# Performance work log

Measured on AMD Instinct MI355X. Metric: run time of the kernel, lower is better.

## Reference

```python
import jax, jax.numpy as jnp
import numpy as np

IN, H, L, B, S = 512, 1024, 6, 64, 256


def setup_inputs() -> dict:
    key = jax.random.key(0)
    ks = jax.random.split(key, 8)
    stdv = 1.0 / np.sqrt(H)
    u = lambda k, shp: jax.random.uniform(k, shp, jnp.float32, -stdv, stdv)
    x = jax.random.normal(ks[0], (B, S, IN), jnp.float32)
    # gate order along last axis of 4H: i, f, c(g), o
    U0 = u(ks[1], (IN, 4 * H))   # layer 0 input weights
    V0 = u(ks[2], (H, 4 * H))    # layer 0 recurrent weights
    b0 = u(ks[3], (4 * H,))
    U = u(ks[4], (L - 1, H, 4 * H))  # layers 1..L-1 input weights
    V = u(ks[5], (L - 1, H, 4 * H))
    b = u(ks[6], (L - 1, 4 * H))
    return {"x": x, "U0": U0, "V0": V0, "b0": b0, "U": U, "V": V, "b": b}


def _cell(xt, h, c, Um, Vm, bm):
    # fused 4-gate GEMM: [B, in] @ [in, 4H] + [B, H] @ [H, 4H]
    z = xt @ Um + h @ Vm + bm
    i, f, g, o = jnp.split(z, 4, axis=-1)
    i = jax.nn.sigmoid(i)
    f = jax.nn.sigmoid(f)
    g = jnp.tanh(g)
    o = jax.nn.sigmoid(o)
    c = f * c + i * g
    h = o * jnp.tanh(c)
    return h, c


def reference(x, U0, V0, b0, U, V, b):
    # Dropout is identity in eval mode (faithful to module.eval()).
    Bb = x.shape[0]
    h0 = jnp.zeros((L, Bb, H), x.dtype)
    c0 = jnp.zeros((L, Bb, H), x.dtype)

    def step(carry, xt):
        h, c = carry
        hs, cs = [], []
        inp = xt
        hn, cn = _cell(inp, h[0], c[0], U0, V0, b0)
        hs.append(hn); cs.append(cn); inp = hn
        for l in range(L - 1):  # fixed small layer loop
            hn, cn = _cell(inp, h[l + 1], c[l + 1], U[l], V[l], b[l])
            hs.append(hn); cs.append(cn); inp = hn
        return (jnp.stack(hs), jnp.stack(cs)), inp

    (hf, cf), seq = jax.lax.scan(step, (h0, c0), jnp.swapaxes(x, 0, 1))
    hidden_seq = jnp.swapaxes(seq, 0, 1)  # [B, S, H]
    return hidden_seq, hf, cf
```

## Files before the change

### kernel.cpp

```cpp
#include <hip/hip_runtime.h>
#include <hip/hip_cooperative_groups.h>

#define B_ 64
#define H_ 1024
#define IN_ 512
#define S_ 256
#define L_ 6
#define NG_ 4096
#define NTASK 768
#define NTICK (S_ + L_ - 1)

typedef __bf16 bf16x8 __attribute__((ext_vector_type(8)));
typedef float f32x4 __attribute__((ext_vector_type(4)));
typedef unsigned short ushort8v __attribute__((ext_vector_type(8)));
typedef unsigned short ushort_t;

#define WP_BYTES 96468992ul
#define XB_BYTES 16777216ul
#define HBF_ELEMS 786432ul
#define LSLOT 65536ul
#define XSLOT 32768ul

__host__ __device__ __forceinline__ size_t poff(int l, int jb) {
  return (l == 0) ? (size_t)jb * 49152ul
                  : 6291456ul + ((size_t)(l - 1) * 128 + jb) * 65536ul;
}

#define MFMA16(a, b, c) __builtin_amdgcn_mfma_f32_16x16x32_bf16(a, b, c, 0, 0, 0)
#define WAITN(n) asm volatile("s_waitcnt vmcnt(" #n ")" ::: "memory")
#define SB0() __builtin_amdgcn_sched_barrier(0)

__device__ __forceinline__ unsigned short f2bf(float f) {
  union { float f; unsigned u; } v; v.f = f;
  unsigned r = v.u + 0x7fffu + ((v.u >> 16) & 1u);
  return (unsigned short)(r >> 16);
}

__global__ void k_pack_w(const float* __restrict__ U0, const float* __restrict__ V0,
                         const float* __restrict__ U, const float* __restrict__ V,
                         ushort_t* __restrict__ Wp) {
  const int bx = blockIdx.x;
  const int l = bx >> 7, jb = bx & 127;
  ushort_t* __restrict__ panel = Wp + poff(l, jb);
  const int KU = (l == 0) ? IN_ : H_;
  const int NU = KU >> 6;
  const int NCH = NU + 16;
  const float* __restrict__ Usrc = (l == 0) ? U0 : U + (size_t)(l - 1) * H_ * NG_;
  const float* __restrict__ Vsrc = (l == 0) ? V0 : V + (size_t)(l - 1) * H_ * NG_;
  const int t = threadIdx.x, lane = t & 63, g4 = t >> 6;
  const int l15 = lane & 15, kg = lane >> 4;
  for (int p = 0; p < NCH; ++p) {
    const int gi = p * 4 + g4;
    const int c = gi >> 2, u = gi & 3, nf = u >> 1, ks = u & 1;
    const int n = (nf * 2 + (l15 >> 3)) * 1024 + jb * 8 + (l15 & 7);
    const int k = c * 64 + ks * 32 + kg * 8;
    const float* __restrict__ src =
        (c < NU) ? (Usrc + (size_t)k * NG_ + n)
                 : (Vsrc + (size_t)(k - KU) * NG_ + n);
    ushort8v uv;
#pragma unroll
    for (int e = 0; e < 8; ++e) uv[e] = f2bf(src[(size_t)e * NG_]);
    *(ushort8v*)(panel + (size_t)gi * 512 + lane * 8) = uv;
  }
}

__global__ void k_cvt_x(const float* __restrict__ x, ushort_t* __restrict__ xb) {
  const int tt = blockIdx.x;
  const int tid = threadIdx.x;
  const int b = tid >> 2, kq = (tid & 3) << 7;
  const float* __restrict__ src = x + ((size_t)b * S_ + tt) * IN_ + kq;
  ushort_t* __restrict__ dst = xb + (size_t)tt * XSLOT;
  const int w = b >> 4, l15 = b & 15;
#pragma unroll
  for (int kk = 0; kk < 128; kk += 8) {
    float4 v0 = *(const float4*)(src + kk);
    float4 v1 = *(const float4*)(src + kk + 4);
    ushort8v u = { f2bf(v0.x), f2bf(v0.y), f2bf(v0.z), f2bf(v0.w),
                   f2bf(v1.x), f2bf(v1.y), f2bf(v1.z), f2bf(v1.w) };
    const int k = kq + kk;
    const int ks = k >> 5, kg = (k & 31) >> 3;
    *(ushort8v*)(dst + (((size_t)ks * 4 + w) * 64 + kg * 16 + l15) * 8) = u;
  }
}

template<int NCH>
__device__ __forceinline__ void gemm_tick(f32x4 acc[2],
                                          const ushort_t* __restrict__ panel,
                                          const ushort_t* __restrict__ A1,
                                          const ushort_t* __restrict__ A2,
                                          int w, int lane) {
  constexpr int NU = NCH - 16;
  bf16x8 Wb[3][4];
  bf16x8 Ab[3][2];
#define LDU(p) (*(const bf16x8*)(p))
#define ISSUE(c) do { \
    const ushort_t* wp_ = panel + (size_t)(c) * 2048 + lane * 8; \
    Wb[(c) % 3][0] = LDU(wp_); \
    Wb[(c) % 3][1] = LDU(wp_ + 512); \
    Wb[(c) % 3][2] = LDU(wp_ + 1024); \
    Wb[(c) % 3][3] = LDU(wp_ + 1536); \
    const ushort_t* ap_ = ((c) < NU \
        ? A1 + ((size_t)(2 * (c)) * 4 + w) * 512 \
        : A2 + ((size_t)(2 * ((c) - NU)) * 4 + w) * 512) + lane * 8; \
    Ab[(c) % 3][0] = LDU(ap_); \
    Ab[(c) % 3][1] = LDU(ap_ + 2048); \
  } while (0)
  ISSUE(0); ISSUE(1); ISSUE(2);
  SB0();
#pragma unroll
  for (int c = 0; c < NCH; ++c) {
    const int rem = NCH - 1 - c;
    if (rem >= 2) { WAITN(12); }
    else if (rem == 1) { WAITN(6); }
    else { WAITN(0); }
    SB0();
    acc[0] = MFMA16(Ab[c % 3][0], Wb[c % 3][0], acc[0]);
    acc[1] = MFMA16(Ab[c % 3][0], Wb[c % 3][2], acc[1]);
    acc[0] = MFMA16(Ab[c % 3][1], Wb[c % 3][1], acc[0]);
    acc[1] = MFMA16(Ab[c % 3][1], Wb[c % 3][3], acc[1]);
    SB0();
    if (c + 3 < NCH) ISSUE(c + 3);
    SB0();
  }
#undef ISSUE
#undef LDU
}

__global__ void __launch_bounds__(256, 3)
k_lstm(const ushort_t* __restrict__ xb,
       const ushort_t* __restrict__ Wp,
       const float* __restrict__ b0,
       const float* __restrict__ bL,
       ushort_t* __restrict__ hbf,
       float* __restrict__ out, int multi) {
  cooperative_groups::grid_group grid = cooperative_groups::this_grid();
  float* __restrict__ seq = out;
  float* __restrict__ hf = out + (size_t)B_ * S_ * H_;
  float* __restrict__ cf = hf + (size_t)L_ * B_ * H_;
  __shared__ float hstF[512];

  const int tid = threadIdx.x;
  const int w = tid >> 6;
  const int lane = tid & 63;
  const int l15 = lane & 15;
  const int kg = lane >> 4;
  const bool lo = (l15 < 8);
  const int wg = blockIdx.x;
  const int nwg = gridDim.x;

  float creg[4] = {0.f, 0.f, 0.f, 0.f};

  for (int T = 0; T < NTICK; ++T) {
    for (int task = wg; task < NTASK; task += nwg) {
      const int l = task >> 7;
      const int jb = task & 127;
      const int t = T - l;
      if (t < 0 || t >= S_) continue;
      const ushort_t* __restrict__ hprev = hbf + (size_t)((T + 1) & 1) * (L_ * LSLOT);
      ushort_t* __restrict__ hcur = hbf + (size_t)(T & 1) * (L_ * LSLOT);
      const ushort_t* __restrict__ panel = Wp + poff(l, jb);
      const ushort_t* __restrict__ A2 = hprev + (size_t)l * LSLOT;

      f32x4 acc[2];
      acc[0] = (f32x4){0.f, 0.f, 0.f, 0.f};
      acc[1] = (f32x4){0.f, 0.f, 0.f, 0.f};
      if (l == 0)
        gemm_tick<24>(acc, panel, xb + (size_t)t * XSLOT, A2, w, lane);
      else
        gemm_tick<32>(acc, panel, hprev + (size_t)(l - 1) * LSLOT, A2, w, lane);

      const int hc = (jb << 3) + (l15 & 7);
      const float* __restrict__ bias = (l == 0) ? b0 : (bL + (size_t)(l - 1) * NG_);
      const float bi = bias[hc];
      const float bfv = bias[1024 + hc];
      const float bgv = bias[2048 + hc];
      const float bov = bias[3072 + hc];

#pragma unroll
      for (int j = 0; j < 4; ++j) {
        float a0 = acc[0][j], a1 = acc[1][j];
        float p0 = __shfl_xor(a0, 8, 64);
        float p1 = __shfl_xor(a1, 8, 64);
        float zi = (lo ? a0 : p0) + bi;
        float zf = (lo ? p0 : a0) + bfv;
        float zg = (lo ? a1 : p1) + bgv;
        float zo = (lo ? p1 : a1) + bov;
        float iv = 1.f / (1.f + expf(-zi));
        float fv = 1.f / (1.f + expf(-zf));
        float gv = tanhf(zg);
        float ov = 1.f / (1.f + expf(-zo));
        const int r = w * 16 + kg * 4 + j;
        float cold;
        if (multi)
          cold = (t > 0) ? cf[((size_t)l * B_ + r) * H_ + hc] : 0.f;
        else
          cold = creg[j];
        float cn = fv * cold + iv * gv;
        creg[j] = cn;
        float hv = ov * tanhf(cn);
        if (lo) {
          hstF[w * 128 + (kg * 4 + j) * 8 + l15] = hv;
          if (multi || t == S_ - 1) cf[((size_t)l * B_ + r) * H_ + hc] = cn;
          if (t == S_ - 1) hf[((size_t)l * B_ + r) * H_ + hc] = hv;
        }
      }
      __syncthreads();
      if (kg == 0) {
        const int lr = l15;
        float4 v0 = *(const float4*)&hstF[w * 128 + lr * 8];
        float4 v1 = *(const float4*)&hstF[w * 128 + lr * 8 + 4];
        ushort8v u8 = { f2bf(v0.x), f2bf(v0.y), f2bf(v0.z), f2bf(v0.w),
                        f2bf(v1.x), f2bf(v1.y), f2bf(v1.z), f2bf(v1.w) };
        *(ushort8v*)(hcur + (size_t)l * LSLOT +
                     (((size_t)(jb >> 2) * 4 + w) * 64 + (jb & 3) * 16 + lr) * 8) = u8;
        if (l == L_ - 1) {
          float* sp = seq + (((size_t)(w * 16 + lr)) * S_ + t) * H_ + (jb << 3);
          *(float4*)sp = v0;
          *(float4*)(sp + 4) = v1;
        }
      }
      __syncthreads();
    }
    grid.sync();
  }
}

extern "C" void kernel_launch(void* const* d_in, const int* in_sizes, int n_in,
                              void* d_out, int out_size, void* d_ws, size_t ws_size,
                              hipStream_t stream) {
  const float* x = (const float*)d_in[0];
  const float* U0 = (const float*)d_in[1];
  const float* V0 = (const float*)d_in[2];
  const float* b0 = (const float*)d_in[3];
  const float* U = (const float*)d_in[4];
  const float* V = (const float*)d_in[5];
  const float* bL = (const float*)d_in[6];
  float* out = (float*)d_out;

  char* ws = (char*)d_ws;
  unsigned short* Wp = (unsigned short*)ws;
  unsigned short* xb = (unsigned short*)(ws + WP_BYTES);
  unsigned short* hbf = (unsigned short*)(ws + WP_BYTES + XB_BYTES);

  hipLaunchKernelGGL(k_pack_w, dim3(NTASK), dim3(256), 0, stream, U0, V0, U, V, Wp);
  hipLaunchKernelGGL(k_cvt_x, dim3(S_), dim3(256), 0, stream, x, xb);
  hipMemsetAsync(hbf, 0, HBF_ELEMS * 2, stream);

  int maxB = 0;
  hipOccupancyMaxActiveBlocksPerMultiprocessor(&maxB, k_lstm, 256, 0);
  int nwg = maxB * 256;
  if (nwg > NTASK) nwg = NTASK;
  if (nwg < 64) nwg = 64;
  int multi = (nwg < NTASK) ? 1 : 0;

  void* args[] = { (void*)&xb, (void*)&Wp, (void*)&b0, (void*)&bL,
                   (void*)&hbf, (void*)&out, (void*)&multi };
  hipError_t e = hipLaunchCooperativeKernel((void*)k_lstm, dim3(nwg), dim3(256),
                                            args, 0, stream);
  if (e != hipSuccess) {
    (void)hipGetLastError();
    nwg = 256; multi = 1;
    void* args2[] = { (void*)&xb, (void*)&Wp, (void*)&b0, (void*)&bL,
                      (void*)&hbf, (void*)&out, (void*)&multi };
    hipLaunchCooperativeKernel((void*)k_lstm, dim3(nwg), dim3(256),
                               args2, 0, stream);
  }
}
```

Measured before the change: 15.17 ms.

## Split K across waves with shared-memory reduction instead of splitting batch rows

Before, each of the four waves handled 16 batch rows and loaded the full weight panel, so every block read the panel four times. Now each wave takes a quarter of the K chunks for all 64 rows and multiplies each weight fragment against four A fragments. The partial sums are reduced through a padded shared-memory buffer, and the gate nonlinearity then runs per (row, 2 hidden units) across all 256 threads. The activation layout and the x conversion kernel are reordered to match. In exchange the block gains a 33 KB shared buffer, an extra reduction pass and more accumulator registers. The occupancy hint in launch bounds is dropped, which may limit how many blocks can be co-resident for the cooperative grid.

```diff
diff --git a/kernel.cpp b/kernel.cpp
--- a/kernel.cpp
+++ b/kernel.cpp
@@ -12,6 +12,7 @@
 
 typedef __bf16 bf16x8 __attribute__((ext_vector_type(8)));
 typedef float f32x4 __attribute__((ext_vector_type(4)));
+typedef float f32x2 __attribute__((ext_vector_type(2)));
 typedef unsigned short ushort8v __attribute__((ext_vector_type(8)));
 typedef unsigned short ushort_t;
 
@@ -70,7 +71,7 @@
   const int b = tid >> 2, kq = (tid & 3) << 7;
   const float* __restrict__ src = x + ((size_t)b * S_ + tt) * IN_ + kq;
   ushort_t* __restrict__ dst = xb + (size_t)tt * XSLOT;
-  const int w = b >> 4, l15 = b & 15;
+  const int m = b >> 4, l15 = b & 15;
 #pragma unroll
   for (int kk = 0; kk < 128; kk += 8) {
     float4 v0 = *(const float4*)(src + kk);
@@ -78,55 +79,64 @@
     ushort8v u = { f2bf(v0.x), f2bf(v0.y), f2bf(v0.z), f2bf(v0.w),
                    f2bf(v1.x), f2bf(v1.y), f2bf(v1.z), f2bf(v1.w) };
     const int k = kq + kk;
-    const int ks = k >> 5, kg = (k & 31) >> 3;
-    *(ushort8v*)(dst + (((size_t)ks * 4 + w) * 64 + kg * 16 + l15) * 8) = u;
+    const int c = k >> 6, ksl = (k >> 5) & 1, kg = (k & 31) >> 3;
+    *(ushort8v*)(dst + (((size_t)c * 8 + m * 2 + ksl) * 64 + kg * 16 + l15) * 8) = u;
   }
 }
 
 template<int NCH>
-__device__ __forceinline__ void gemm_tick(f32x4 acc[2],
-                                          const ushort_t* __restrict__ panel,
-                                          const ushort_t* __restrict__ A1,
-                                          const ushort_t* __restrict__ A2,
-                                          int w, int lane) {
+__device__ __forceinline__ void gemm_q(f32x4 acc[4][2],
+                                       const ushort_t* __restrict__ panel,
+                                       const ushort_t* __restrict__ A1,
+                                       const ushort_t* __restrict__ A2,
+                                       int w, int lane) {
   constexpr int NU = NCH - 16;
-  bf16x8 Wb[3][4];
-  bf16x8 Ab[3][2];
+  constexpr int Q = NCH / 4;
+  bf16x8 Wb[2][4];
+  bf16x8 Ab[2][8];
 #define LDU(p) (*(const bf16x8*)(p))
-#define ISSUE(c) do { \
+#define ISSUE(c, bk) do { \
     const ushort_t* wp_ = panel + (size_t)(c) * 2048 + lane * 8; \
-    Wb[(c) % 3][0] = LDU(wp_); \
-    Wb[(c) % 3][1] = LDU(wp_ + 512); \
-    Wb[(c) % 3][2] = LDU(wp_ + 1024); \
-    Wb[(c) % 3][3] = LDU(wp_ + 1536); \
+    Wb[bk][0] = LDU(wp_); \
+    Wb[bk][1] = LDU(wp_ + 512); \
+    Wb[bk][2] = LDU(wp_ + 1024); \
+    Wb[bk][3] = LDU(wp_ + 1536); \
     const ushort_t* ap_ = ((c) < NU \
-        ? A1 + ((size_t)(2 * (c)) * 4 + w) * 512 \
-        : A2 + ((size_t)(2 * ((c) - NU)) * 4 + w) * 512) + lane * 8; \
-    Ab[(c) % 3][0] = LDU(ap_); \
-    Ab[(c) % 3][1] = LDU(ap_ + 2048); \
+        ? A1 + (size_t)(c) * 4096 : A2 + (size_t)((c) - NU) * 4096) + lane * 8; \
+    Ab[bk][0] = LDU(ap_); \
+    Ab[bk][1] = LDU(ap_ + 512); \
+    Ab[bk][2] = LDU(ap_ + 1024); \
+    Ab[bk][3] = LDU(ap_ + 1536); \
+    Ab[bk][4] = LDU(ap_ + 2048); \
+    Ab[bk][5] = LDU(ap_ + 2560); \
+    Ab[bk][6] = LDU(ap_ + 3072); \
+    Ab[bk][7] = LDU(ap_ + 3584); \
   } while (0)
-  ISSUE(0); ISSUE(1); ISSUE(2);
+  const int c0 = w * Q;
+  ISSUE(c0, 0);
+  if (Q > 1) ISSUE(c0 + 1, 1);
   SB0();
 #pragma unroll
-  for (int c = 0; c < NCH; ++c) {
-    const int rem = NCH - 1 - c;
-    if (rem >= 2) { WAITN(12); }
-    else if (rem == 1) { WAITN(6); }
-    else { WAITN(0); }
+  for (int j = 0; j < Q; ++j) {
+    if (j + 1 < Q) { WAITN(12); } else { WAITN(0); }
     SB0();
-    acc[0] = MFMA16(Ab[c % 3][0], Wb[c % 3][0], acc[0]);
-    acc[1] = MFMA16(Ab[c % 3][0], Wb[c % 3][2], acc[1]);
-    acc[0] = MFMA16(Ab[c % 3][1], Wb[c % 3][1], acc[0]);
-    acc[1] = MFMA16(Ab[c % 3][1], Wb[c % 3][3], acc[1]);
+    const int bk = j & 1;
+#pragma unroll
+    for (int ks = 0; ks < 2; ++ks)
+#pragma unroll
+      for (int m = 0; m < 4; ++m) {
+        acc[m][0] = MFMA16(Ab[bk][m * 2 + ks], Wb[bk][ks], acc[m][0]);
+        acc[m][1] = MFMA16(Ab[bk][m * 2 + ks], Wb[bk][2 + ks], acc[m][1]);
+      }
     SB0();
-    if (c + 3 < NCH) ISSUE(c + 3);
+    if (j + 2 < Q) ISSUE(c0 + j + 2, bk);
     SB0();
   }
 #undef ISSUE
 #undef LDU
 }
 
-__global__ void __launch_bounds__(256, 3)
+__global__ void __launch_bounds__(256)
 k_lstm(const ushort_t* __restrict__ xb,
        const ushort_t* __restrict__ Wp,
        const float* __restrict__ b0,
@@ -137,6 +147,7 @@
   float* __restrict__ seq = out;
   float* __restrict__ hf = out + (size_t)B_ * S_ * H_;
   float* __restrict__ cf = hf + (size_t)L_ * B_ * H_;
+  __shared__ float zsp[4][64][33];
   __shared__ float hstF[512];
 
   const int tid = threadIdx.x;
@@ -144,11 +155,12 @@
   const int lane = tid & 63;
   const int l15 = lane & 15;
   const int kg = lane >> 4;
-  const bool lo = (l15 < 8);
   const int wg = blockIdx.x;
   const int nwg = gridDim.x;
 
-  float creg[4] = {0.f, 0.f, 0.f, 0.f};
+  const int grow = tid >> 2;
+  const int gq = (tid & 3) << 1;
+  float creg[2] = {0.f, 0.f};
 
   for (int T = 0; T < NTICK; ++T) {
     for (int task = wg; task < NTASK; task += nwg) {
@@ -157,67 +169,79 @@
       const int t = T - l;
       if (t < 0 || t >= S_) continue;
       const ushort_t* __restrict__ hprev = hbf + (size_t)((T + 1) & 1) * (L_ * LSLOT);
-      ushort_t* __restrict__ hcur = hbf + (size_t)(T & 1) * (L_ * LSLOT);
+      ushort_t* __restrict__ hcur = hbf + (size_t)(T & 1) * (L_ * LSLOT) + (size_t)l * LSLOT;
       const ushort_t* __restrict__ panel = Wp + poff(l, jb);
       const ushort_t* __restrict__ A2 = hprev + (size_t)l * LSLOT;
 
-      f32x4 acc[2];
-      acc[0] = (f32x4){0.f, 0.f, 0.f, 0.f};
-      acc[1] = (f32x4){0.f, 0.f, 0.f, 0.f};
+      f32x4 acc[4][2];
+#pragma unroll
+      for (int m = 0; m < 4; ++m) {
+        acc[m][0] = (f32x4){0.f, 0.f, 0.f, 0.f};
+        acc[m][1] = (f32x4){0.f, 0.f, 0.f, 0.f};
+      }
       if (l == 0)
-        gemm_tick<24>(acc, panel, xb + (size_t)t * XSLOT, A2, w, lane);
+        gemm_q<24>(acc, panel, xb + (size_t)t * XSLOT, A2, w, lane);
       else
-        gemm_tick<32>(acc, panel, hprev + (size_t)(l - 1) * LSLOT, A2, w, lane);
-
-      const int hc = (jb << 3) + (l15 & 7);
-      const float* __restrict__ bias = (l == 0) ? b0 : (bL + (size_t)(l - 1) * NG_);
-      const float bi = bias[hc];
-      const float bfv = bias[1024 + hc];
-      const float bgv = bias[2048 + hc];
-      const float bov = bias[3072 + hc];
-
-#pragma unroll
-      for (int j = 0; j < 4; ++j) {
-        float a0 = acc[0][j], a1 = acc[1][j];
-        float p0 = __shfl_xor(a0, 8, 64);
-        float p1 = __shfl_xor(a1, 8, 64);
-        float zi = (lo ? a0 : p0) + bi;
-        float zf = (lo ? p0 : a0) + bfv;
-        float zg = (lo ? a1 : p1) + bgv;
-        float zo = (lo ? p1 : a1) + bov;
-        float iv = 1.f / (1.f + expf(-zi));
-        float fv = 1.f / (1.f + expf(-zf));
-        float gv = tanhf(zg);
-        float ov = 1.f / (1.f + expf(-zo));
-        const int r = w * 16 + kg * 4 + j;
-        float cold;
-        if (multi)
-          cold = (t > 0) ? cf[((size_t)l * B_ + r) * H_ + hc] : 0.f;
-        else
-          cold = creg[j];
-        float cn = fv * cold + iv * gv;
-        creg[j] = cn;
-        float hv = ov * tanhf(cn);
-        if (lo) {
-          hstF[w * 128 + (kg * 4 + j) * 8 + l15] = hv;
-          if (multi || t == S_ - 1) cf[((size_t)l * B_ + r) * H_ + hc] = cn;
-          if (t == S_ - 1) hf[((size_t)l * B_ + r) * H_ + hc] = hv;
+        gemm_q<32>(acc, panel, hprev + (size_t)(l - 1) * LSLOT, A2, w, lane);
+
+#pragma unroll
+      for (int m = 0; m < 4; ++m)
+#pragma unroll
+        for (int nf = 0; nf < 2; ++nf)
+#pragma unroll
+          for (int j = 0; j < 4; ++j)
+            zsp[w][m * 16 + kg * 4 + j][nf * 16 + l15] = acc[m][nf][j];
+      __syncthreads();
+
+      {
+        const int hc0 = (jb << 3) + gq;
+        const float* __restrict__ bias = (l == 0) ? b0 : (bL + (size_t)(l - 1) * NG_);
+        const size_t cbase = ((size_t)l * B_ + grow) * H_ + hc0;
+        f32x2 cold;
+        if (multi) {
+          if (t > 0) cold = *(const f32x2*)(cf + cbase);
+          else cold = (f32x2){0.f, 0.f};
+        } else {
+          cold = (f32x2){creg[0], creg[1]};
         }
+        f32x2 hv2, cn2;
+#pragma unroll
+        for (int q = 0; q < 2; ++q) {
+          const int hcl = gq + q;
+          float z[4];
+#pragma unroll
+          for (int g = 0; g < 4; ++g) {
+            const int c32 = (g >> 1) * 16 + (g & 1) * 8 + hcl;
+            z[g] = zsp[0][grow][c32] + zsp[1][grow][c32] +
+                   zsp[2][grow][c32] + zsp[3][grow][c32] +
+                   bias[g * 1024 + hc0 + q];
+          }
+          float iv = 1.f / (1.f + expf(-z[0]));
+          float fv = 1.f / (1.f + expf(-z[1]));
+          float gv = tanhf(z[2]);
+          float ov = 1.f / (1.f + expf(-z[3]));
+          float cn = fv * cold[q] + iv * gv;
+          cn2[q] = cn;
+          creg[q] = cn;
+          float hv = ov * tanhf(cn);
+          hv2[q] = hv;
+          hstF[grow * 8 + hcl] = hv;
+        }
+        if (multi || t == S_ - 1) *(f32x2*)(cf + cbase) = cn2;
+        if (t == S_ - 1) *(f32x2*)(hf + cbase) = hv2;
+        if (l == L_ - 1)
+          *(f32x2*)(seq + ((size_t)grow * S_ + t) * H_ + hc0) = hv2;
       }
       __syncthreads();
-      if (kg == 0) {
-        const int lr = l15;
-        float4 v0 = *(const float4*)&hstF[w * 128 + lr * 8];
-        float4 v1 = *(const float4*)&hstF[w * 128 + lr * 8 + 4];
-        ushort8v u8 = { f2bf(v0.x), f2bf(v0.y), f2bf(v0.z), f2bf(v0.w),
-                        f2bf(v1.x), f2bf(v1.y), f2bf(v1.z), f2bf(v1.w) };
-        *(ushort8v*)(hcur + (size_t)l * LSLOT +
-                     (((size_t)(jb >> 2) * 4 + w) * 64 + (jb & 3) * 16 + lr) * 8) = u8;
-        if (l == L_ - 1) {
-          float* sp = seq + (((size_t)(w * 16 + lr)) * S_ + t) * H_ + (jb << 3);
-          *(float4*)sp = v0;
-          *(float4*)(sp + 4) = v1;
-        }
+
+      if (tid < 64) {
+        const int m = tid >> 4, lr = tid & 15;
+        const float* hp = &hstF[(m * 16 + lr) * 8];
+        ushort8v u8 = { f2bf(hp[0]), f2bf(hp[1]), f2bf(hp[2]), f2bf(hp[3]),
+                        f2bf(hp[4]), f2bf(hp[5]), f2bf(hp[6]), f2bf(hp[7]) };
+        *(ushort8v*)(hcur +
+                     (((size_t)(jb >> 3) * 8 + m * 2 + ((jb >> 2) & 1)) * 64 +
+                      ((jb & 3) * 16 + lr)) * 8) = u8;
       }
       __syncthreads();
     }
```

Result: faster. 13.56 ms (-10.6%).
